# Kernel optimization log

Measured on AMD Instinct MI355X. Metric: run time of the kernel, lower is better.

Reference implementation:

```python
import jax, jax.numpy as jnp
import numpy as np

D_MODEL = 1024
D_STATE = 128
D_CONV = 4
EXPAND = 2
HEADDIM = 64
D_INNER = EXPAND * D_MODEL          # 2048
NHEADS = D_INNER // HEADDIM         # 32
NGROUPS = 1
CONV_DIM = D_INNER + 2 * NGROUPS * D_STATE            # 2304
D_IN_PROJ = 2 * D_INNER + 2 * NGROUPS * D_STATE + NHEADS  # 4384
NUM_CLASS = 48
BATCH = 2
SEQLEN = 512


def setup_inputs() -> dict:
    key = jax.random.key(0)
    ks = jax.random.split(key, 8)
    s = 0.02
    inputs = jax.random.normal(ks[0], (BATCH, SEQLEN, D_MODEL), jnp.float32)
    W_in = jax.random.normal(ks[1], (D_MODEL, D_IN_PROJ), jnp.float32) * s
    conv_w = jax.random.normal(ks[2], (CONV_DIM, D_CONV), jnp.float32) * 0.2
    conv_b = jnp.zeros((CONV_DIM,), jnp.float32)
    # dt_bias = inverse-softplus of dt sampled in [1e-3, 0.1] (mamba init)
    dt = jnp.exp(jax.random.uniform(ks[3], (NHEADS,), jnp.float32) * (np.log(0.1) - np.log(1e-3)) + np.log(1e-3))
    dt_bias = dt + jnp.log(-jnp.expm1(-dt))
    A_log = jnp.log(jax.random.uniform(ks[4], (NHEADS,), jnp.float32, 1.0, 16.0))
    D = jnp.ones((NHEADS,), jnp.float32)
    norm_w = jnp.ones((D_INNER,), jnp.float32)
    W_out = jax.random.normal(ks[5], (D_INNER, D_MODEL), jnp.float32) * s
    W_cls = jax.random.normal(ks[6], (D_INNER, NUM_CLASS), jnp.float32) * s
    b_cls = jnp.zeros((NUM_CLASS,), jnp.float32)
    return {"inputs": inputs, "W_in": W_in, "conv_w": conv_w, "conv_b": conv_b,
            "dt_bias": dt_bias, "A_log": A_log, "D": D, "norm_w": norm_w,
            "W_out": W_out, "W_cls": W_cls, "b_cls": b_cls}


def _forward(inputs, W_in, conv_w, conv_b, dt_bias, A_log, D, norm_w, W_out, W_cls, b_cls):
    B, L, _ = inputs.shape
    zxbcdt = inputs @ W_in                                     # (B,L,4384)
    z, xBC, dt = jnp.split(zxbcdt, [D_INNER, D_INNER + CONV_DIM], axis=-1)
    dt = jax.nn.softplus(dt + dt_bias)                         # (B,L,H)
    # causal depthwise conv over time on (x,B,C)
    xBC_t = jnp.pad(jnp.transpose(xBC, (0, 2, 1)), ((0, 0), (0, 0), (D_CONV - 1, 0)))
    xBC_c = jax.lax.conv_general_dilated(xBC_t, conv_w[:, None, :], (1,), 'VALID',
                                         feature_group_count=CONV_DIM)
    xBC = jax.nn.silu(jnp.transpose(xBC_c, (0, 2, 1)) + conv_b)
    x, Bm, Cm = jnp.split(xBC, [D_INNER, D_INNER + D_STATE], axis=-1)
    x = x.reshape(B, L, NHEADS, HEADDIM)
    A = -jnp.exp(A_log)                                        # (H,)
    dA = jnp.exp(dt * A)                                       # (B,L,H)

    def step(state, inp):
        # state: (B,H,P,N) -- selective SSM recurrence (chunk_size=1 path)
        x_t, B_t, C_t, dt_t, dA_t = inp
        state = state * dA_t[:, :, None, None] + jnp.einsum('bhp,bn,bh->bhpn', x_t, B_t, dt_t)
        y_t = jnp.einsum('bhpn,bn->bhp', state, C_t)
        return state, y_t

    state0 = jnp.zeros((B, NHEADS, HEADDIM, D_STATE), inputs.dtype)
    xs = (jnp.transpose(x, (1, 0, 2, 3)), jnp.transpose(Bm, (1, 0, 2)),
          jnp.transpose(Cm, (1, 0, 2)), jnp.transpose(dt, (1, 0, 2)),
          jnp.transpose(dA, (1, 0, 2)))
    _, ys = jax.lax.scan(step, state0, xs)                     # ys: (L,B,H,P)
    y = jnp.transpose(ys, (1, 0, 2, 3)) + D[None, None, :, None] * x
    y = y.reshape(B, L, D_INNER)
    # gated RMSNorm: rmsnorm(y * silu(z)) * weight
    y = y * jax.nn.silu(z)
    y = y * jax.lax.rsqrt(jnp.mean(y * y, axis=-1, keepdims=True) + 1e-5) * norm_w
    # hidden_states (d_inner=2048) go through the per-timestep classifier
    preds = y @ W_cls + b_cls                                  # (B,L,num_class)
    return preds


def reference(inputs, W_in, conv_w, conv_b, dt_bias, A_log, D, norm_w, W_out, W_cls, b_cls):
    return _forward(inputs, W_in, conv_w, conv_b, dt_bias, A_log, D, norm_w, W_out, W_cls, b_cls)
```

## Files before the change

kernel.cpp:

```cpp
#include <hip/hip_runtime.h>
#include <hip/hip_bf16.h>
#include <cstdint>

#define BATCH 2
#define SEQLEN 512
#define BL (BATCH*SEQLEN)
#define DMODEL 1024
#define DINNER 2048
#define NHEADS 32
#define HEADDIM 64
#define DSTATE 128
#define CONVDIM 2304
#define DINPROJ 4384
#define NCLS 48
#define QC 64
#define NCH 8

typedef short bf16x8 __attribute__((ext_vector_type(8)));
typedef float f32x4  __attribute__((ext_vector_type(4)));

static __device__ __forceinline__ unsigned short f2bf(float f) {
    unsigned u = __float_as_uint(f);
    unsigned r = (u + 0x7FFFu + ((u >> 16) & 1u)) >> 16;
    return (unsigned short)r;
}

__global__ __launch_bounds__(256) void k_cvt_a(const float* __restrict__ in,
                                               unsigned short* __restrict__ out) {
    int i = (blockIdx.x * 256 + threadIdx.x) * 4;
    float4 v = *(const float4*)(in + i);
    ushort4 o;
    o.x = f2bf(v.x); o.y = f2bf(v.y); o.z = f2bf(v.z); o.w = f2bf(v.w);
    *(ushort4*)(out + i) = o;
}

__global__ __launch_bounds__(256) void k_transpose_w(const float* __restrict__ W,
                                                     unsigned short* __restrict__ Wt) {
    __shared__ float tile[32][33];
    int n0 = blockIdx.x * 32;
    int k0 = blockIdx.y * 32;
    int tx = threadIdx.x & 31;
    int ty = threadIdx.x >> 5;
#pragma unroll
    for (int i = 0; i < 4; ++i) {
        int k = k0 + ty + i * 8;
        tile[ty + i * 8][tx] = W[(size_t)k * DINPROJ + n0 + tx];
    }
    __syncthreads();
#pragma unroll
    for (int i = 0; i < 4; ++i) {
        int n = n0 + ty + i * 8;
        Wt[(size_t)n * DMODEL + k0 + tx] = f2bf(tile[tx][ty + i * 8]);
    }
}

__global__ __launch_bounds__(256) void k_cvt_wcls(const float* __restrict__ W,
                                                  unsigned short* __restrict__ Wt) {
    int n = blockIdx.x;
    for (int k = threadIdx.x; k < DINNER; k += 256)
        Wt[(size_t)n * DINNER + k] = f2bf(W[(size_t)k * NCLS + n]);
}

__global__ __launch_bounds__(256) void k_gemm_in(const unsigned short* __restrict__ A,
                                                 const unsigned short* __restrict__ Bt,
                                                 float* __restrict__ C) {
    __shared__ unsigned short As[128][40];
    __shared__ unsigned short Bs[64][40];
    const int tid  = threadIdx.x;
    const int m0   = blockIdx.y * 128;
    const int n0   = blockIdx.x * 64;
    const int lr   = tid >> 2;
    const int lc   = (tid & 3) * 8;
    const int wv   = tid >> 6;
    const int lane = tid & 63;
    const int fr   = lane & 15;
    const int fk   = (lane >> 4) * 8;
    f32x4 acc[2][4] = {};
    for (int k0 = 0; k0 < DMODEL; k0 += 32) {
        __syncthreads();
        *(uint4*)(&As[lr][lc])      = *(const uint4*)(A + (size_t)(m0 + lr) * DMODEL + k0 + lc);
        *(uint4*)(&As[lr + 64][lc]) = *(const uint4*)(A + (size_t)(m0 + lr + 64) * DMODEL + k0 + lc);
        int n = n0 + lr;
        uint4 bv = make_uint4(0u, 0u, 0u, 0u);
        if (n < DINPROJ) bv = *(const uint4*)(Bt + (size_t)n * DMODEL + k0 + lc);
        *(uint4*)(&Bs[lr][lc]) = bv;
        __syncthreads();
        bf16x8 af0 = *(const bf16x8*)(&As[wv * 32 + fr][fk]);
        bf16x8 af1 = *(const bf16x8*)(&As[wv * 32 + 16 + fr][fk]);
        bf16x8 bfr[4];
#pragma unroll
        for (int nt = 0; nt < 4; ++nt) bfr[nt] = *(const bf16x8*)(&Bs[nt * 16 + fr][fk]);
#pragma unroll
        for (int nt = 0; nt < 4; ++nt) {
            acc[0][nt] = __builtin_amdgcn_mfma_f32_16x16x32_bf16(af0, bfr[nt], acc[0][nt], 0, 0, 0);
            acc[1][nt] = __builtin_amdgcn_mfma_f32_16x16x32_bf16(af1, bfr[nt], acc[1][nt], 0, 0, 0);
        }
    }
    const int r4 = (lane >> 4) * 4;
#pragma unroll
    for (int mt = 0; mt < 2; ++mt) {
#pragma unroll
        for (int nt = 0; nt < 4; ++nt) {
            int col = n0 + nt * 16 + fr;
            if (col < DINPROJ) {
#pragma unroll
                for (int r = 0; r < 4; ++r) {
                    int row = m0 + wv * 32 + mt * 16 + r4 + r;
                    C[(size_t)row * DINPROJ + col] = acc[mt][nt][r];
                }
            }
        }
    }
}

__global__ __launch_bounds__(256) void k_conv_dt(const float* __restrict__ zx,
                                                 const float* __restrict__ conv_w,
                                                 const float* __restrict__ conv_b,
                                                 const float* __restrict__ dt_bias,
                                                 float* __restrict__ xbc,
                                                 float* __restrict__ dtb) {
    int row = blockIdx.y;
    int c   = blockIdx.x * 256 + threadIdx.x;
    int b = row >> 9, l = row & 511;
    if (c < CONVDIM) {
        float acc = conv_b[c];
#pragma unroll
        for (int j = 0; j < 4; ++j) {
            int ls = l - 3 + j;
            float v = (ls >= 0) ? zx[((size_t)(b * SEQLEN + ls)) * DINPROJ + DINNER + c] : 0.f;
            acc += v * conv_w[c * 4 + j];
        }
        float s = acc / (1.f + expf(-acc));
        xbc[(size_t)row * CONVDIM + c] = s;
    } else if (c < CONVDIM + NHEADS) {
        int h = c - CONVDIM;
        float raw = zx[(size_t)row * DINPROJ + (DINNER + CONVDIM) + h] + dt_bias[h];
        float dt = (raw > 20.f) ? raw : log1pf(expf(raw));
        dtb[row * NHEADS + h] = dt;
    }
}

__global__ __launch_bounds__(256) void k_chunk(const float* __restrict__ xbc,
                                               const float* __restrict__ dtb,
                                               const float* __restrict__ A_log,
                                               const float* __restrict__ Dvec,
                                               float* __restrict__ yb,
                                               float* __restrict__ Sc_g,
                                               float* __restrict__ lam_g,
                                               float* __restrict__ esc_g) {
    const int gid = blockIdx.x;
    const int c = gid & 7;
    const int h = (gid >> 3) & 31;
    const int b = gid >> 8;
    const int row0 = b * SEQLEN + c * QC;

    __shared__ float cumS[QC], wS[QC], dtS[QC];
    __shared__ unsigned short Xt[QC][72];
    __shared__ unsigned short Bs[QC][136];
    __shared__ unsigned short BtW[DSTATE][72];
    __shared__ unsigned short Cs[QC][136];
    __shared__ unsigned short Gs[QC][72];

    const int tid = threadIdx.x;
    if (tid < 64) {
        float dtv = dtb[(size_t)(row0 + tid) * NHEADS + h];
        float nA = -expf(A_log[h]);
        float x = dtv * nA;
#pragma unroll
        for (int off = 1; off < 64; off <<= 1) {
            float v = __shfl_up(x, off, 64);
            if (tid >= off) x += v;
        }
        float cumTot = __shfl(x, 63, 64);
        cumS[tid] = x;
        dtS[tid] = dtv;
        wS[tid] = expf(cumTot - x) * dtv;
        esc_g[(size_t)gid * QC + tid] = expf(x);
        if (tid == 0) lam_g[gid] = expf(cumTot);
    }
    __syncthreads();

    {
        int row = tid >> 2;
        int g = tid & 3;
        const float* rp = xbc + (size_t)(row0 + row) * CONVDIM;
        float wrow = wS[row];
#pragma unroll
        for (int i = 0; i < 4; ++i) {
            float4 v = *(const float4*)(rp + h * HEADDIM + g * 16 + i * 4);
            int p = g * 16 + i * 4;
            Xt[p + 0][row] = f2bf(v.x);
            Xt[p + 1][row] = f2bf(v.y);
            Xt[p + 2][row] = f2bf(v.z);
            Xt[p + 3][row] = f2bf(v.w);
        }
#pragma unroll
        for (int i = 0; i < 8; ++i) {
            int n = g * 32 + i * 4;
            float4 v = *(const float4*)(rp + DINNER + n);
            ushort4 u;
            u.x = f2bf(v.x); u.y = f2bf(v.y); u.z = f2bf(v.z); u.w = f2bf(v.w);
            *(ushort4*)(&Bs[row][n]) = u;
            BtW[n + 0][row] = f2bf(v.x * wrow);
            BtW[n + 1][row] = f2bf(v.y * wrow);
            BtW[n + 2][row] = f2bf(v.z * wrow);
            BtW[n + 3][row] = f2bf(v.w * wrow);
        }
#pragma unroll
        for (int i = 0; i < 8; ++i) {
            int n = g * 32 + i * 4;
            float4 v = *(const float4*)(rp + DINNER + DSTATE + n);
            ushort4 u;
            u.x = f2bf(v.x); u.y = f2bf(v.y); u.z = f2bf(v.z); u.w = f2bf(v.w);
            *(ushort4*)(&Cs[row][n]) = u;
        }
    }
    __syncthreads();

    const int w = tid >> 6, lane = tid & 63;
    const int fr = lane & 15, fq = lane >> 4, fk = (lane >> 4) * 8;

    f32x4 accG[4] = {};
#pragma unroll
    for (int kk = 0; kk < 4; ++kk) {
        bf16x8 a = *(const bf16x8*)(&Cs[w * 16 + fr][kk * 32 + fk]);
#pragma unroll
        for (int nt = 0; nt < 4; ++nt) {
            bf16x8 bb = *(const bf16x8*)(&Bs[nt * 16 + fr][kk * 32 + fk]);
            accG[nt] = __builtin_amdgcn_mfma_f32_16x16x32_bf16(a, bb, accG[nt], 0, 0, 0);
        }
    }
#pragma unroll
    for (int nt = 0; nt < 4; ++nt) {
        int s = nt * 16 + fr;
        float cs = cumS[s], dts = dtS[s];
#pragma unroll
        for (int r = 0; r < 4; ++r) {
            int t = w * 16 + fq * 4 + r;
            float val = (s <= t) ? accG[nt][r] * expf(cumS[t] - cs) * dts : 0.f;
            Gs[t][s] = f2bf(val);
        }
    }
    __syncthreads();

    f32x4 accY[4] = {};
#pragma unroll
    for (int kk = 0; kk < 2; ++kk) {
        bf16x8 a = *(const bf16x8*)(&Gs[w * 16 + fr][kk * 32 + fk]);
#pragma unroll
        for (int pt = 0; pt < 4; ++pt) {
            bf16x8 bb = *(const bf16x8*)(&Xt[pt * 16 + fr][kk * 32 + fk]);
            accY[pt] = __builtin_amdgcn_mfma_f32_16x16x32_bf16(a, bb, accY[pt], 0, 0, 0);
        }
    }
    f32x4 accS[8] = {};
#pragma unroll
    for (int kk = 0; kk < 2; ++kk) {
        bf16x8 a = *(const bf16x8*)(&Xt[w * 16 + fr][kk * 32 + fk]);
#pragma unroll
        for (int nt = 0; nt < 8; ++nt) {
            bf16x8 bb = *(const bf16x8*)(&BtW[nt * 16 + fr][kk * 32 + fk]);
            accS[nt] = __builtin_amdgcn_mfma_f32_16x16x32_bf16(a, bb, accS[nt], 0, 0, 0);
        }
    }
    float Dh = Dvec[h];
#pragma unroll
    for (int pt = 0; pt < 4; ++pt) {
        int p = pt * 16 + fr;
#pragma unroll
        for (int r = 0; r < 4; ++r) {
            int t = w * 16 + fq * 4 + r;
            float xv = xbc[(size_t)(row0 + t) * CONVDIM + h * HEADDIM + p];
            yb[(size_t)(row0 + t) * DINNER + h * HEADDIM + p] = accY[pt][r] + Dh * xv;
        }
    }
    float* scp = Sc_g + (size_t)gid * (HEADDIM * DSTATE);
#pragma unroll
    for (int nt = 0; nt < 8; ++nt) {
        int n = nt * 16 + fr;
#pragma unroll
        for (int r = 0; r < 4; ++r) {
            int p = w * 16 + fq * 4 + r;
            scp[p * DSTATE + n] = accS[nt][r];
        }
    }
}

__global__ __launch_bounds__(256) void k_chain(const float* __restrict__ Sc_g,
                                               const float* __restrict__ lam_g,
                                               unsigned short* __restrict__ Sin_bf) {
    int bh = blockIdx.x;
    int tid = threadIdx.x;
    float s[32];
#pragma unroll
    for (int i = 0; i < 32; ++i) s[i] = 0.f;
    for (int c = 0; c < NCH; ++c) {
        size_t base = (size_t)(bh * NCH + c) * (HEADDIM * DSTATE) + tid * 32;
#pragma unroll
        for (int j = 0; j < 32; j += 4) {
            ushort4 u;
            u.x = f2bf(s[j + 0]); u.y = f2bf(s[j + 1]);
            u.z = f2bf(s[j + 2]); u.w = f2bf(s[j + 3]);
            *(ushort4*)(Sin_bf + base + j) = u;
        }
        float lam = lam_g[bh * NCH + c];
#pragma unroll
        for (int j = 0; j < 32; j += 4) {
            float4 v = *(const float4*)(Sc_g + base + j);
            s[j + 0] = s[j + 0] * lam + v.x;
            s[j + 1] = s[j + 1] * lam + v.y;
            s[j + 2] = s[j + 2] * lam + v.z;
            s[j + 3] = s[j + 3] * lam + v.w;
        }
    }
}

__global__ __launch_bounds__(256) void k_cross(const float* __restrict__ xbc,
                                               const float* __restrict__ esc_g,
                                               const unsigned short* __restrict__ Sin_bf,
                                               float* __restrict__ yb) {
    const int gid = blockIdx.x;
    const int c = gid & 7;
    const int h = (gid >> 3) & 31;
    const int b = gid >> 8;
    const int row0 = b * SEQLEN + c * QC;
    __shared__ unsigned short Ct[QC][136];
    __shared__ unsigned short Ss[QC][136];
    const int tid = threadIdx.x;
    {
        int row = tid >> 2, g = tid & 3;
        const float* rp = xbc + (size_t)(row0 + row) * CONVDIM + DINNER + DSTATE;
        float esc = esc_g[(size_t)gid * QC + row];
#pragma unroll
        for (int i = 0; i < 8; ++i) {
            int n = g * 32 + i * 4;
            float4 v = *(const float4*)(rp + n);
            ushort4 u;
            u.x = f2bf(v.x * esc); u.y = f2bf(v.y * esc);
            u.z = f2bf(v.z * esc); u.w = f2bf(v.w * esc);
            *(ushort4*)(&Ct[row][n]) = u;
        }
        const uint4* sp = (const uint4*)(Sin_bf + (size_t)gid * (HEADDIM * DSTATE));
#pragma unroll
        for (int i = 0; i < 4; ++i) {
            uint4 v = sp[row * 16 + g * 4 + i];
            *(uint4*)(&Ss[row][g * 32 + i * 8]) = v;
        }
    }
    __syncthreads();
    const int w = tid >> 6, lane = tid & 63;
    const int fr = lane & 15, fq = lane >> 4, fk = (lane >> 4) * 8;
    f32x4 acc[4] = {};
#pragma unroll
    for (int kk = 0; kk < 4; ++kk) {
        bf16x8 a = *(const bf16x8*)(&Ct[w * 16 + fr][kk * 32 + fk]);
#pragma unroll
        for (int pt = 0; pt < 4; ++pt) {
            bf16x8 bb = *(const bf16x8*)(&Ss[pt * 16 + fr][kk * 32 + fk]);
            acc[pt] = __builtin_amdgcn_mfma_f32_16x16x32_bf16(a, bb, acc[pt], 0, 0, 0);
        }
    }
#pragma unroll
    for (int pt = 0; pt < 4; ++pt) {
        int p = pt * 16 + fr;
#pragma unroll
        for (int r = 0; r < 4; ++r) {
            int t = w * 16 + fq * 4 + r;
            size_t yi = (size_t)(row0 + t) * DINNER + h * HEADDIM + p;
            yb[yi] += acc[pt][r];
        }
    }
}

__global__ __launch_bounds__(256) void k_gate_norm(const float* __restrict__ zx,
                                                   const float* __restrict__ nw,
                                                   const float* __restrict__ y,
                                                   unsigned short* __restrict__ Gbf) {
    int row = blockIdx.x;
    int tid = threadIdx.x;
    const float* zrow = zx + (size_t)row * DINPROJ;
    const float* yr = y + (size_t)row * DINNER;
    float g[8];
    float ss = 0.f;
#pragma unroll
    for (int i = 0; i < 2; ++i) {
        int c = tid * 4 + i * 1024;
        float4 yv = *(const float4*)(yr + c);
        float4 zv = *(const float4*)(zrow + c);
        float zs[4] = {zv.x, zv.y, zv.z, zv.w};
        float ys[4] = {yv.x, yv.y, yv.z, yv.w};
#pragma unroll
        for (int k = 0; k < 4; ++k) {
            float sil = zs[k] / (1.f + expf(-zs[k]));
            float gg = ys[k] * sil;
            g[i * 4 + k] = gg;
            ss += gg * gg;
        }
    }
#pragma unroll
    for (int off = 32; off >= 1; off >>= 1) ss += __shfl_xor(ss, off, 64);
    __shared__ float wsum[4];
    if ((tid & 63) == 0) wsum[tid >> 6] = ss;
    __syncthreads();
    float tot = wsum[0] + wsum[1] + wsum[2] + wsum[3];
    float scale = rsqrtf(tot / (float)DINNER + 1e-5f);
#pragma unroll
    for (int i = 0; i < 2; ++i) {
        int c = tid * 4 + i * 1024;
        float4 nv = *(const float4*)(nw + c);
        ushort4 o;
        o.x = f2bf(g[i * 4 + 0] * scale * nv.x);
        o.y = f2bf(g[i * 4 + 1] * scale * nv.y);
        o.z = f2bf(g[i * 4 + 2] * scale * nv.z);
        o.w = f2bf(g[i * 4 + 3] * scale * nv.w);
        *(ushort4*)(Gbf + (size_t)row * DINNER + c) = o;
    }
}

__global__ __launch_bounds__(256) void k_init_out(const float* __restrict__ bcls,
                                                  float* __restrict__ out) {
    int i = blockIdx.x * 256 + threadIdx.x;
    out[i] = bcls[i % NCLS];
}

__global__ __launch_bounds__(256) void k_cls_mfma(const unsigned short* __restrict__ G,
                                                  const unsigned short* __restrict__ Wt,
                                                  float* __restrict__ out) {
    __shared__ unsigned short Gs[64][72];
    __shared__ unsigned short Ws[48][72];
    const int m0  = blockIdx.x * 64;
    const int k00 = blockIdx.y * 256;
    const int tid = threadIdx.x;
    const int w = tid >> 6, lane = tid & 63;
    const int fr = lane & 15, fq = lane >> 4, fk = fq * 8;
    f32x4 acc[3] = {};
    for (int ks = 0; ks < 4; ++ks) {
        int k0 = k00 + ks * 64;
        __syncthreads();
        {
            int row = tid >> 2, seg = (tid & 3) * 16;
            const unsigned short* gp = G + (size_t)(m0 + row) * DINNER + k0 + seg;
            *(uint4*)(&Gs[row][seg])     = *(const uint4*)(gp);
            *(uint4*)(&Gs[row][seg + 8]) = *(const uint4*)(gp + 8);
        }
        if (tid < 192) {
            int row = tid >> 2, seg = (tid & 3) * 16;
            const unsigned short* wp = Wt + (size_t)row * DINNER + k0 + seg;
            *(uint4*)(&Ws[row][seg])     = *(const uint4*)(wp);
            *(uint4*)(&Ws[row][seg + 8]) = *(const uint4*)(wp + 8);
        }
        __syncthreads();
#pragma unroll
        for (int kk = 0; kk < 2; ++kk) {
            bf16x8 a = *(const bf16x8*)(&Gs[w * 16 + fr][kk * 32 + fk]);
#pragma unroll
            for (int nt = 0; nt < 3; ++nt) {
                bf16x8 bb = *(const bf16x8*)(&Ws[nt * 16 + fr][kk * 32 + fk]);
                acc[nt] = __builtin_amdgcn_mfma_f32_16x16x32_bf16(a, bb, acc[nt], 0, 0, 0);
            }
        }
    }
#pragma unroll
    for (int nt = 0; nt < 3; ++nt) {
        int col = nt * 16 + fr;
#pragma unroll
        for (int r = 0; r < 4; ++r) {
            int row = m0 + w * 16 + fq * 4 + r;
            atomicAdd(&out[(size_t)row * NCLS + col], acc[nt][r]);
        }
    }
}

extern "C" void kernel_launch(void* const* d_in, const int* in_sizes, int n_in,
                              void* d_out, int out_size, void* d_ws, size_t ws_size,
                              hipStream_t stream) {
    const float* inputs  = (const float*)d_in[0];
    const float* W_in    = (const float*)d_in[1];
    const float* conv_w  = (const float*)d_in[2];
    const float* conv_b  = (const float*)d_in[3];
    const float* dt_bias = (const float*)d_in[4];
    const float* A_log   = (const float*)d_in[5];
    const float* Dvec    = (const float*)d_in[6];
    const float* norm_w  = (const float*)d_in[7];
    const float* W_cls   = (const float*)d_in[9];
    const float* b_cls   = (const float*)d_in[10];
    float* out = (float*)d_out;

    float* ws   = (float*)d_ws;
    float* zx   = ws;
    float* xbc  = zx   + (size_t)BL * DINPROJ;
    float* dtb  = xbc  + (size_t)BL * CONVDIM;
    float* yb   = dtb  + (size_t)BL * NHEADS;
    float* Sc_g = yb   + (size_t)BL * DINNER;
    float* lam_g= Sc_g + (size_t)BATCH * NHEADS * NCH * HEADDIM * DSTATE;
    float* esc_g= lam_g+ (size_t)BATCH * NHEADS * NCH;
    unsigned short* Sin_bf = (unsigned short*)(esc_g + (size_t)BATCH * NHEADS * NCH * QC);
    unsigned short* abf    = Sin_bf + (size_t)BATCH * NHEADS * NCH * HEADDIM * DSTATE;
    unsigned short* wtbf   = abf + (size_t)BL * DMODEL;
    unsigned short* wclsbf = wtbf + (size_t)DINPROJ * DMODEL;
    unsigned short* Gbf    = (unsigned short*)Sc_g;

    k_cvt_a<<<dim3(BL * DMODEL / (256 * 4)), dim3(256), 0, stream>>>(inputs, abf);
    k_transpose_w<<<dim3(DINPROJ / 32, DMODEL / 32), dim3(256), 0, stream>>>(W_in, wtbf);
    k_cvt_wcls<<<dim3(NCLS), dim3(256), 0, stream>>>(W_cls, wclsbf);
    k_gemm_in<<<dim3((DINPROJ + 63) / 64, BL / 128), dim3(256), 0, stream>>>(abf, wtbf, zx);
    k_conv_dt<<<dim3(10, BL), dim3(256), 0, stream>>>(zx, conv_w, conv_b, dt_bias, xbc, dtb);
    k_chunk<<<dim3(BATCH * NHEADS * NCH), dim3(256), 0, stream>>>(xbc, dtb, A_log, Dvec,
                                                                  yb, Sc_g, lam_g, esc_g);
    k_chain<<<dim3(BATCH * NHEADS), dim3(256), 0, stream>>>(Sc_g, lam_g, Sin_bf);
    k_cross<<<dim3(BATCH * NHEADS * NCH), dim3(256), 0, stream>>>(xbc, esc_g, Sin_bf, yb);
    k_gate_norm<<<dim3(BL), dim3(256), 0, stream>>>(zx, norm_w, yb, Gbf);
    k_init_out<<<dim3(BL * NCLS / 256), dim3(256), 0, stream>>>(b_cls, out);
    k_cls_mfma<<<dim3(BL / 64, 8), dim3(256), 0, stream>>>(Gbf, wclsbf, out);
}
```

Baseline: 191.3 us.

## Enlarge in-proj GEMM tile to 128x128 with direct global-to-LDS loads

The input-projection GEMM moves from 128x64 block tiles to 128x128 tiles. Each wave now computes a 64x64 sub-tile of 4x4 MFMAs, and operands are loaded with global_load_lds straight into unpadded shared memory. The N dimension is padded to 4480, with the extra output columns masked on store. This is meant to raise data reuse per LDS load and cut register staging, at the cost of fewer blocks (280) and possible LDS bank conflicts from the unpadded layout. Separately, the bias init of the output and the W_cls conversion are merged into one kernel to save a launch.

```diff
diff --git a/kernel.cpp b/kernel.cpp
--- a/kernel.cpp
+++ b/kernel.cpp
@@ -12,12 +12,20 @@
 #define DSTATE 128
 #define CONVDIM 2304
 #define DINPROJ 4384
+#define NPROJPAD 4480
 #define NCLS 48
 #define QC 64
 #define NCH 8
 
 typedef short bf16x8 __attribute__((ext_vector_type(8)));
 typedef float f32x4  __attribute__((ext_vector_type(4)));
+typedef unsigned int u32;
+typedef const __attribute__((address_space(1))) u32 gu32;
+typedef __attribute__((address_space(3))) u32 lu32;
+
+static __device__ __forceinline__ void gl16(const void* g, void* l) {
+    __builtin_amdgcn_global_load_lds((gu32*)g, (lu32*)l, 16, 0, 0);
+}
 
 static __device__ __forceinline__ unsigned short f2bf(float f) {
     unsigned u = __float_as_uint(f);
@@ -54,58 +62,74 @@
     }
 }
 
-__global__ __launch_bounds__(256) void k_cvt_wcls(const float* __restrict__ W,
-                                                  unsigned short* __restrict__ Wt) {
-    int n = blockIdx.x;
-    for (int k = threadIdx.x; k < DINNER; k += 256)
-        Wt[(size_t)n * DINNER + k] = f2bf(W[(size_t)k * NCLS + n]);
+__global__ __launch_bounds__(256) void k_prep_cls(const float* __restrict__ W,
+                                                  const float* __restrict__ bcls,
+                                                  unsigned short* __restrict__ Wt,
+                                                  float* __restrict__ out) {
+    int bid = blockIdx.x;
+    if (bid < 192) {
+        int i = bid * 256 + threadIdx.x;
+        out[i] = bcls[i % NCLS];
+    } else {
+        int n = bid - 192;
+        for (int k = threadIdx.x; k < DINNER; k += 256)
+            Wt[(size_t)n * DINNER + k] = f2bf(W[(size_t)k * NCLS + n]);
+    }
 }
 
 __global__ __launch_bounds__(256) void k_gemm_in(const unsigned short* __restrict__ A,
                                                  const unsigned short* __restrict__ Bt,
                                                  float* __restrict__ C) {
-    __shared__ unsigned short As[128][40];
-    __shared__ unsigned short Bs[64][40];
+    __shared__ unsigned short As[128 * 32];
+    __shared__ unsigned short Bs[128 * 32];
     const int tid  = threadIdx.x;
     const int m0   = blockIdx.y * 128;
-    const int n0   = blockIdx.x * 64;
-    const int lr   = tid >> 2;
-    const int lc   = (tid & 3) * 8;
-    const int wv   = tid >> 6;
+    const int n0   = blockIdx.x * 128;
+    const int w    = tid >> 6;
     const int lane = tid & 63;
-    const int fr   = lane & 15;
-    const int fk   = (lane >> 4) * 8;
-    f32x4 acc[2][4] = {};
+    const int wm   = w >> 1, wn = w & 1;
+    const int fr   = lane & 15, fq = lane >> 4;
+    const int srow = w * 16 + (lane >> 2);
+    const int skg  = (lane & 3) * 8;
+    const unsigned short* gA0 = A  + (size_t)(m0 + srow) * DMODEL + skg;
+    const unsigned short* gA1 = gA0 + (size_t)64 * DMODEL;
+    const unsigned short* gB0 = Bt + (size_t)(n0 + srow) * DMODEL + skg;
+    const unsigned short* gB1 = gB0 + (size_t)64 * DMODEL;
+    unsigned short* lA0 = As + w * 512;
+    unsigned short* lA1 = As + 2048 + w * 512;
+    unsigned short* lB0 = Bs + w * 512;
+    unsigned short* lB1 = Bs + 2048 + w * 512;
+
+    f32x4 acc[4][4] = {};
     for (int k0 = 0; k0 < DMODEL; k0 += 32) {
         __syncthreads();
-        *(uint4*)(&As[lr][lc])      = *(const uint4*)(A + (size_t)(m0 + lr) * DMODEL + k0 + lc);
-        *(uint4*)(&As[lr + 64][lc]) = *(const uint4*)(A + (size_t)(m0 + lr + 64) * DMODEL + k0 + lc);
-        int n = n0 + lr;
-        uint4 bv = make_uint4(0u, 0u, 0u, 0u);
-        if (n < DINPROJ) bv = *(const uint4*)(Bt + (size_t)n * DMODEL + k0 + lc);
-        *(uint4*)(&Bs[lr][lc]) = bv;
+        gl16(gA0 + k0, lA0);
+        gl16(gA1 + k0, lA1);
+        gl16(gB0 + k0, lB0);
+        gl16(gB1 + k0, lB1);
         __syncthreads();
-        bf16x8 af0 = *(const bf16x8*)(&As[wv * 32 + fr][fk]);
-        bf16x8 af1 = *(const bf16x8*)(&As[wv * 32 + 16 + fr][fk]);
-        bf16x8 bfr[4];
-#pragma unroll
-        for (int nt = 0; nt < 4; ++nt) bfr[nt] = *(const bf16x8*)(&Bs[nt * 16 + fr][fk]);
+        bf16x8 af[4], bf[4];
+#pragma unroll
+        for (int mt = 0; mt < 4; ++mt)
+            af[mt] = *(const bf16x8*)(&As[(wm * 64 + mt * 16 + fr) * 32 + fq * 8]);
+#pragma unroll
+        for (int nt = 0; nt < 4; ++nt)
+            bf[nt] = *(const bf16x8*)(&Bs[(wn * 64 + nt * 16 + fr) * 32 + fq * 8]);
+#pragma unroll
+        for (int mt = 0; mt < 4; ++mt)
+#pragma unroll
+            for (int nt = 0; nt < 4; ++nt)
+                acc[mt][nt] = __builtin_amdgcn_mfma_f32_16x16x32_bf16(af[mt], bf[nt], acc[mt][nt], 0, 0, 0);
+    }
+#pragma unroll
+    for (int mt = 0; mt < 4; ++mt) {
 #pragma unroll
         for (int nt = 0; nt < 4; ++nt) {
-            acc[0][nt] = __builtin_amdgcn_mfma_f32_16x16x32_bf16(af0, bfr[nt], acc[0][nt], 0, 0, 0);
-            acc[1][nt] = __builtin_amdgcn_mfma_f32_16x16x32_bf16(af1, bfr[nt], acc[1][nt], 0, 0, 0);
-        }
-    }
-    const int r4 = (lane >> 4) * 4;
-#pragma unroll
-    for (int mt = 0; mt < 2; ++mt) {
-#pragma unroll
-        for (int nt = 0; nt < 4; ++nt) {
-            int col = n0 + nt * 16 + fr;
+            int col = n0 + wn * 64 + nt * 16 + fr;
             if (col < DINPROJ) {
 #pragma unroll
                 for (int r = 0; r < 4; ++r) {
-                    int row = m0 + wv * 32 + mt * 16 + r4 + r;
+                    int row = m0 + wm * 64 + mt * 16 + fq * 4 + r;
                     C[(size_t)row * DINPROJ + col] = acc[mt][nt][r];
                 }
             }
@@ -415,12 +439,6 @@
         o.w = f2bf(g[i * 4 + 3] * scale * nv.w);
         *(ushort4*)(Gbf + (size_t)row * DINNER + c) = o;
     }
-}
-
-__global__ __launch_bounds__(256) void k_init_out(const float* __restrict__ bcls,
-                                                  float* __restrict__ out) {
-    int i = blockIdx.x * 256 + threadIdx.x;
-    out[i] = bcls[i % NCLS];
 }
 
 __global__ __launch_bounds__(256) void k_cls_mfma(const unsigned short* __restrict__ G,
@@ -497,19 +515,18 @@
     unsigned short* Sin_bf = (unsigned short*)(esc_g + (size_t)BATCH * NHEADS * NCH * QC);
     unsigned short* abf    = Sin_bf + (size_t)BATCH * NHEADS * NCH * HEADDIM * DSTATE;
     unsigned short* wtbf   = abf + (size_t)BL * DMODEL;
-    unsigned short* wclsbf = wtbf + (size_t)DINPROJ * DMODEL;
+    unsigned short* wclsbf = wtbf + (size_t)NPROJPAD * DMODEL;
     unsigned short* Gbf    = (unsigned short*)Sc_g;
 
     k_cvt_a<<<dim3(BL * DMODEL / (256 * 4)), dim3(256), 0, stream>>>(inputs, abf);
     k_transpose_w<<<dim3(DINPROJ / 32, DMODEL / 32), dim3(256), 0, stream>>>(W_in, wtbf);
-    k_cvt_wcls<<<dim3(NCLS), dim3(256), 0, stream>>>(W_cls, wclsbf);
-    k_gemm_in<<<dim3((DINPROJ + 63) / 64, BL / 128), dim3(256), 0, stream>>>(abf, wtbf, zx);
+    k_prep_cls<<<dim3(240), dim3(256), 0, stream>>>(W_cls, b_cls, wclsbf, out);
+    k_gemm_in<<<dim3(NPROJPAD / 128, BL / 128), dim3(256), 0, stream>>>(abf, wtbf, zx);
     k_conv_dt<<<dim3(10, BL), dim3(256), 0, stream>>>(zx, conv_w, conv_b, dt_bias, xbc, dtb);
     k_chunk<<<dim3(BATCH * NHEADS * NCH), dim3(256), 0, stream>>>(xbc, dtb, A_log, Dvec,
                                                                   yb, Sc_g, lam_g, esc_g);
     k_chain<<<dim3(BATCH * NHEADS), dim3(256), 0, stream>>>(Sc_g, lam_g, Sin_bf);
     k_cross<<<dim3(BATCH * NHEADS * NCH), dim3(256), 0, stream>>>(xbc, esc_g, Sin_bf, yb);
     k_gate_norm<<<dim3(BL), dim3(256), 0, stream>>>(zx, norm_w, yb, Gbf);
-    k_init_out<<<dim3(BL * NCLS / 256), dim3(256), 0, stream>>>(b_cls, out);
     k_cls_mfma<<<dim3(BL / 64, 8), dim3(256), 0, stream>>>(Gbf, wclsbf, out);
 }
```

After: 184.1 us. 3.7% less time.
